# Kernel optimization log

Hardware: AMD Instinct MI355X
Metric: run time of the kernel (lower is better)

## Reference

```python
import jax, jax.numpy as jnp
import numpy as np
import math

DROPOUT_P = 0.1

def setup_inputs() -> dict:
    key = jax.random.key(0)
    k1, k2, k3 = jax.random.split(key, 3)
    B, Lq, Lk, D = 8, 2048, 2048, 128
    x1 = jax.random.normal(k1, (B, Lq, D), dtype=jnp.float32)
    x2 = jax.random.normal(k2, (B, Lk, D), dtype=jnp.float32)
    qm = jnp.zeros((1, Lq, Lk), dtype=jnp.float32)  # additive attention mask
    u = jax.random.uniform(k3, (B, Lq, Lk), dtype=jnp.float32)  # dropout uniforms
    return {"x1": x1, "x2": x2, "qm": qm, "u": u}

def reference(x1, x2, qm, u):
    # scaled dot-product attention with additive mask + inverted dropout
    scale = 1.0 / math.sqrt(x1.shape[-1])
    qk = jnp.einsum('bqd,bkd->bqk', x1, x2) * scale + qm  # [B, Lq, Lk]
    attn = jax.nn.softmax(qk, axis=-1)
    keep = (u >= DROPOUT_P).astype(attn.dtype) / (1.0 - DROPOUT_P)
    attn = attn * keep
    out = jnp.einsum('bqk,bkd->bqd', attn, x2)  # [B, Lq, D]
    return out
```

## Files before the change

### kernel.cpp

```cpp
#include <hip/hip_runtime.h>
#include <hip/hip_bf16.h>
#include <stdint.h>

#define LQ 2048
#define LK 2048
#define DH 128
#define BQ 64
#define KB 128
#define NT (LK / KB)
#define KROW 136
#define LOG2E 1.44269504088896340736f
#define QSCALE 0.088388347648318447f

typedef __attribute__((ext_vector_type(8)))  short bf16x8;
typedef __attribute__((ext_vector_type(16))) float f32x16;
typedef __attribute__((ext_vector_type(4)))  float f32x4;

union FragAB { uint32_t u[4]; bf16x8 v; };

__device__ __forceinline__ uint32_t pack2_bf16(float lo, float hi) {
  union { __hip_bfloat16 b; uint16_t u; } a, c;
  a.b = __float2bfloat16(lo);
  c.b = __float2bfloat16(hi);
  return (uint32_t)a.u | ((uint32_t)c.u << 16);
}

__device__ __forceinline__ void stage_writes(uint16_t* Kb, uint16_t* Vb,
                                             const f32x4* st, int sbi, int sbj) {
#pragma unroll
  for (int j = 0; j < 2; ++j) {
    const int rowb = 4 * (sbi + 16 * j);
#pragma unroll
    for (int r = 0; r < 4; ++r) {
      uint32_t* kw = (uint32_t*)(Kb + (size_t)(rowb + r) * KROW + 4 * sbj);
      f32x4 v = st[j * 4 + r];
      kw[0] = pack2_bf16(v.x, v.y);
      kw[1] = pack2_bf16(v.z, v.w);
    }
#pragma unroll
    for (int c = 0; c < 4; ++c) {
      uint32_t* vw = (uint32_t*)(Vb + (size_t)(4 * sbj + c) * KROW + rowb);
      vw[0] = pack2_bf16(st[j * 4 + 0][c], st[j * 4 + 1][c]);
      vw[1] = pack2_bf16(st[j * 4 + 2][c], st[j * 4 + 3][c]);
    }
  }
}

__global__ __launch_bounds__(512, 2)
void fattn_kernel(const float* __restrict__ x1, const float* __restrict__ x2,
                  const float* __restrict__ qm, const float* __restrict__ uu,
                  float* __restrict__ out)
{
  __shared__ uint16_t ldsK[2][128 * KROW];
  __shared__ uint16_t ldsV[2][128 * KROW];

  const int tid  = threadIdx.x;
  const int wv   = tid >> 6;
  const int lane = tid & 63;
  const int ln   = lane & 31;
  const int h    = lane >> 5;
  const int qsub = wv & 1;
  const int ks   = wv >> 1;

  const int b    = blockIdx.x & 7;
  const int qblk = blockIdx.x >> 3;
  const int qrow = qblk * BQ + qsub * 32 + ln;

  FragAB qf[8];
  {
    const float* qp = x1 + ((size_t)(b * LQ + qrow)) * DH + h * 8;
    const float qs = QSCALE * LOG2E;
#pragma unroll
    for (int dc = 0; dc < 8; ++dc) {
      f32x4 a = *(const f32x4*)(qp + dc * 16);
      f32x4 c = *(const f32x4*)(qp + dc * 16 + 4);
      qf[dc].u[0] = pack2_bf16(a.x * qs, a.y * qs);
      qf[dc].u[1] = pack2_bf16(a.z * qs, a.w * qs);
      qf[dc].u[2] = pack2_bf16(c.x * qs, c.y * qs);
      qf[dc].u[3] = pack2_bf16(c.z * qs, c.w * qs);
    }
  }

  const int sbi = tid >> 5;
  const int sbj = tid & 31;
  const float* x2base = x2 + (size_t)b * LK * DH + sbj * 4;
  const float* ubase  = uu + ((size_t)(b * LQ + qrow)) * LK + ks * 32 + h * 4;
  const float* qmbase = qm + ((size_t)qrow) * LK + ks * 32 + h * 4;

  f32x4 st[8];
#pragma unroll
  for (int j = 0; j < 2; ++j)
#pragma unroll
    for (int r = 0; r < 4; ++r)
      st[j * 4 + r] = *(const f32x4*)(x2base + (size_t)(4 * (sbi + 16 * j) + r) * DH);

  f32x4 ucur[4];
#pragma unroll
  for (int g = 0; g < 4; ++g)
    ucur[g] = __builtin_nontemporal_load((const f32x4*)(ubase + g * 8));

  stage_writes(ldsK[0], ldsV[0], st, sbi, sbj);
  __syncthreads();

  float m_run = -1e30f, l_run = 0.f;
  f32x16 acco[4];
#pragma unroll
  for (int d2 = 0; d2 < 4; ++d2)
#pragma unroll
    for (int i = 0; i < 16; ++i) acco[d2][i] = 0.f;

  for (int t = 0; t < NT; ++t) {
    const int cb = t & 1;
    const uint16_t* Kb = ldsK[cb];
    const uint16_t* Vb = ldsV[cb];
    const int kb = t * KB;

    f32x4 qmv[4];
#pragma unroll
    for (int g = 0; g < 4; ++g)
      qmv[g] = *(const f32x4*)(qmbase + (size_t)kb + g * 8);

    f32x4 unext[4];
    if (t + 1 < NT) {
#pragma unroll
      for (int j = 0; j < 2; ++j)
#pragma unroll
        for (int r = 0; r < 4; ++r)
          st[j * 4 + r] = *(const f32x4*)(x2base + (size_t)(kb + KB + 4 * (sbi + 16 * j) + r) * DH);
#pragma unroll
      for (int g = 0; g < 4; ++g)
        unext[g] = __builtin_nontemporal_load((const f32x4*)(ubase + (size_t)(kb + KB) + g * 8));
    }

    f32x16 sacc;
#pragma unroll
    for (int i = 0; i < 16; ++i) sacc[i] = 0.f;
    const uint16_t* Krow = Kb + (size_t)(ks * 32 + ln) * KROW + h * 8;
#pragma unroll
    for (int dc = 0; dc < 8; ++dc) {
      bf16x8 af = *(const bf16x8*)(Krow + dc * 16);
      sacc = __builtin_amdgcn_mfma_f32_32x32x16_bf16(af, qf[dc].v, sacc, 0, 0, 0);
    }

#pragma unroll
    for (int g = 0; g < 4; ++g)
#pragma unroll
      for (int j2 = 0; j2 < 4; ++j2)
        sacc[g * 4 + j2] += qmv[g][j2] * LOG2E;
    float pm = sacc[0];
#pragma unroll
    for (int i = 1; i < 16; ++i) pm = fmaxf(pm, sacc[i]);
    pm = fmaxf(pm, __shfl_xor(pm, 32));
    const float mnew = fmaxf(m_run, pm);
    const float resc = __builtin_amdgcn_exp2f(m_run - mnew);
    m_run = mnew;
    float rs = 0.f;
#pragma unroll
    for (int i = 0; i < 16; ++i) {
      sacc[i] = __builtin_amdgcn_exp2f(sacc[i] - mnew);
      rs += sacc[i];
    }
    rs += __shfl_xor(rs, 32);
    l_run = l_run * resc + rs;

#pragma unroll
    for (int g = 0; g < 4; ++g)
#pragma unroll
      for (int j2 = 0; j2 < 4; ++j2)
        sacc[g * 4 + j2] = (ucur[g][j2] >= 0.1f) ? sacc[g * 4 + j2] : 0.f;

    uint32_t pr[4][2], sw[4][2];
#pragma unroll
    for (int g = 0; g < 4; ++g) {
      pr[g][0] = pack2_bf16(sacc[4 * g + 0], sacc[4 * g + 1]);
      pr[g][1] = pack2_bf16(sacc[4 * g + 2], sacc[4 * g + 3]);
      sw[g][0] = __shfl_xor(pr[g][0], 32);
      sw[g][1] = __shfl_xor(pr[g][1], 32);
    }
    FragAB bfr[2];
#pragma unroll
    for (int c = 0; c < 2; ++c) {
      bfr[c].u[0] = h ? sw[2 * c + 1][0] : pr[2 * c][0];
      bfr[c].u[1] = h ? sw[2 * c + 1][1] : pr[2 * c][1];
      bfr[c].u[2] = h ? pr[2 * c + 1][0] : sw[2 * c][0];
      bfr[c].u[3] = h ? pr[2 * c + 1][1] : sw[2 * c][1];
    }

#pragma unroll
    for (int d2 = 0; d2 < 4; ++d2)
#pragma unroll
      for (int i = 0; i < 16; ++i) acco[d2][i] *= resc;

#pragma unroll
    for (int d2 = 0; d2 < 4; ++d2) {
      const uint16_t* Vrow = Vb + (size_t)(d2 * 32 + ln) * KROW + ks * 32 + h * 8;
#pragma unroll
      for (int c = 0; c < 2; ++c) {
        bf16x8 av = *(const bf16x8*)(Vrow + c * 16);
        acco[d2] = __builtin_amdgcn_mfma_f32_32x32x16_bf16(av, bfr[c].v, acco[d2], 0, 0, 0);
      }
    }

    if (t + 1 < NT) {
      stage_writes(ldsK[cb ^ 1], ldsV[cb ^ 1], st, sbi, sbj);
#pragma unroll
      for (int g = 0; g < 4; ++g) ucur[g] = unext[g];
    }
    __syncthreads();
  }

  float* scr = (wv < 4) ? ((float*)ldsK + (size_t)wv * 4224)
                        : ((float*)ldsV + (size_t)(wv - 4) * 4224);
  scr[lane]      = m_run;
  scr[64 + lane] = l_run;
#pragma unroll
  for (int d2 = 0; d2 < 4; ++d2)
#pragma unroll
    for (int g = 0; g < 4; ++g) {
      f32x4 vv;
#pragma unroll
      for (int j2 = 0; j2 < 4; ++j2) vv[j2] = acco[d2][g * 4 + j2];
      *(f32x4*)(scr + 128 + (size_t)(d2 * 4 + g) * 256 + lane * 4) = vv;
    }
  __syncthreads();

  if (wv < 2) {
    const float* rg[4];
#pragma unroll
    for (int s2 = 0; s2 < 4; ++s2) {
      const int r = qsub + 2 * s2;
      rg[s2] = (r < 4) ? ((const float*)ldsK + (size_t)r * 4224)
                       : ((const float*)ldsV + (size_t)(r - 4) * 4224);
    }
    const float ms0 = rg[0][lane], ms1 = rg[1][lane], ms2 = rg[2][lane], ms3 = rg[3][lane];
    const float ls0 = rg[0][64 + lane], ls1 = rg[1][64 + lane];
    const float ls2 = rg[2][64 + lane], ls3 = rg[3][64 + lane];
    const float mM = fmaxf(fmaxf(ms0, ms1), fmaxf(ms2, ms3));
    const float e0 = __builtin_amdgcn_exp2f(ms0 - mM);
    const float e1 = __builtin_amdgcn_exp2f(ms1 - mM);
    const float e2 = __builtin_amdgcn_exp2f(ms2 - mM);
    const float e3 = __builtin_amdgcn_exp2f(ms3 - mM);
    const float lM = e0 * ls0 + e1 * ls1 + e2 * ls2 + e3 * ls3;
    const float inv = (1.0f / 0.9f) / lM;
    float* op = out + ((size_t)(b * LQ + qrow)) * DH;
#pragma unroll
    for (int d2 = 0; d2 < 4; ++d2)
#pragma unroll
      for (int g = 0; g < 4; ++g) {
        const size_t off = 128 + (size_t)(d2 * 4 + g) * 256 + lane * 4;
        f32x4 a4 = e0 * *(const f32x4*)(rg[0] + off)
                 + e1 * *(const f32x4*)(rg[1] + off)
                 + e2 * *(const f32x4*)(rg[2] + off)
                 + e3 * *(const f32x4*)(rg[3] + off);
        a4 = a4 * inv;
        *(f32x4*)(op + d2 * 32 + 8 * g + 4 * h) = a4;
      }
  }
}

extern "C" void kernel_launch(void* const* d_in, const int* in_sizes, int n_in,
                              void* d_out, int out_size, void* d_ws, size_t ws_size,
                              hipStream_t stream) {
  (void)in_sizes; (void)n_in; (void)out_size; (void)d_ws; (void)ws_size;
  const float* x1 = (const float*)d_in[0];
  const float* x2 = (const float*)d_in[1];
  const float* qm = (const float*)d_in[2];
  const float* u  = (const float*)d_in[3];
  float* out = (float*)d_out;
  dim3 grid(256), block(512);
  fattn_kernel<<<grid, block, 0, stream>>>(x1, x2, qm, u, out);
}
```

Before: 257.5 us.

## Precompute dropout bitmask and bf16 transposed mask in prepass kernels

Two new prepass kernels run before attention. One packs the float dropout uniforms into a bit mask using wave ballots, and the other converts the additive mask into pre-scaled bf16 in a transposed layout matched to the MFMA fragments. The attention kernel then reads a single 32-bit word per tile for dropout and two 16-byte loads for the mask, replacing many scattered fp32 loads in the inner loop. The cost is two extra launches and a full read of the uniforms tensor in the prepass. Separately, the LDS staging writes are merged into 64-bit stores, and the mask is rounded to bf16, which loses some precision.

```diff
diff --git a/kernel.cpp b/kernel.cpp
--- a/kernel.cpp
+++ b/kernel.cpp
@@ -25,6 +25,58 @@
   return (uint32_t)a.u | ((uint32_t)c.u << 16);
 }
 
+__global__ __launch_bounds__(256)
+void mask_kernel(const float* __restrict__ uu, uint32_t* __restrict__ maskp) {
+  const int lane = threadIdx.x & 63;
+  const int wid  = blockIdx.x * 4 + (threadIdx.x >> 6);
+#pragma unroll 1
+  for (int i = 0; i < 16; ++i) {
+    const size_t F = ((size_t)i * 8192 + wid) * 256;
+    float u0 = uu[F + 0 * 64 + lane];
+    float u1 = uu[F + 1 * 64 + lane];
+    float u2 = uu[F + 2 * 64 + lane];
+    float u3 = uu[F + 3 * 64 + lane];
+    uint64_t B0 = __ballot(u0 >= 0.1f);
+    uint64_t B1 = __ballot(u1 >= 0.1f);
+    uint64_t B2 = __ballot(u2 >= 0.1f);
+    uint64_t B3 = __ballot(u3 >= 0.1f);
+    if (lane < 8) {
+      const int m = lane;
+      uint64_t bb = (m < 2) ? B0 : (m < 4) ? B1 : (m < 6) ? B2 : B3;
+      uint32_t val = (m & 1) ? (uint32_t)(bb >> 32) : (uint32_t)bb;
+      const size_t row = F >> 11;
+      const int c = (int)((F >> 5) & 63) + m;
+      maskp[row * 64 + (size_t)((c & 3) * 16 + (c >> 2))] = val;
+    }
+  }
+}
+
+__global__ __launch_bounds__(256)
+void qmt_kernel(const float* __restrict__ qm, uint16_t* __restrict__ qmt2) {
+  const int kc = threadIdx.x & 63;
+  const int q  = blockIdx.x * 4 + (threadIdx.x >> 6);
+  f32x4 r[8];
+  const float* src = qm + (size_t)q * 2048 + kc * 32;
+#pragma unroll
+  for (int c = 0; c < 8; ++c) r[c] = *(const f32x4*)(src + c * 4);
+#pragma unroll
+  for (int h = 0; h < 2; ++h) {
+    uint32_t w[8];
+#pragma unroll
+    for (int i = 0; i < 8; ++i) {
+      const int gi0 = 2 * i, gi1 = 2 * i + 1;
+      const float v0 = r[h + (gi0 >> 2) * 2][gi0 & 3] * LOG2E;
+      const float v1 = r[h + (gi1 >> 2) * 2][gi1 & 3] * LOG2E;
+      w[i] = pack2_bf16(v0, v1);
+    }
+    uint16_t* dst = qmt2 + ((size_t)(kc * 2 + h) * 2048 + q) * 16;
+    uint4 lo = {w[0], w[1], w[2], w[3]};
+    uint4 hi = {w[4], w[5], w[6], w[7]};
+    *(uint4*)dst = lo;
+    *(uint4*)(dst + 8) = hi;
+  }
+}
+
 __device__ __forceinline__ void stage_writes(uint16_t* Kb, uint16_t* Vb,
                                              const f32x4* st, int sbi, int sbj) {
 #pragma unroll
@@ -32,23 +84,24 @@
     const int rowb = 4 * (sbi + 16 * j);
 #pragma unroll
     for (int r = 0; r < 4; ++r) {
-      uint32_t* kw = (uint32_t*)(Kb + (size_t)(rowb + r) * KROW + 4 * sbj);
       f32x4 v = st[j * 4 + r];
-      kw[0] = pack2_bf16(v.x, v.y);
-      kw[1] = pack2_bf16(v.z, v.w);
+      uint64_t pk = (uint64_t)pack2_bf16(v.x, v.y) |
+                    ((uint64_t)pack2_bf16(v.z, v.w) << 32);
+      *(uint64_t*)(Kb + (size_t)(rowb + r) * KROW + 4 * sbj) = pk;
     }
 #pragma unroll
     for (int c = 0; c < 4; ++c) {
-      uint32_t* vw = (uint32_t*)(Vb + (size_t)(4 * sbj + c) * KROW + rowb);
-      vw[0] = pack2_bf16(st[j * 4 + 0][c], st[j * 4 + 1][c]);
-      vw[1] = pack2_bf16(st[j * 4 + 2][c], st[j * 4 + 3][c]);
+      uint64_t pv = (uint64_t)pack2_bf16(st[j * 4 + 0][c], st[j * 4 + 1][c]) |
+                    ((uint64_t)pack2_bf16(st[j * 4 + 2][c], st[j * 4 + 3][c]) << 32);
+      *(uint64_t*)(Vb + (size_t)(4 * sbj + c) * KROW + rowb) = pv;
     }
   }
 }
 
 __global__ __launch_bounds__(512, 2)
 void fattn_kernel(const float* __restrict__ x1, const float* __restrict__ x2,
-                  const float* __restrict__ qm, const float* __restrict__ uu,
+                  const uint32_t* __restrict__ maskp,
+                  const uint16_t* __restrict__ qmt2,
                   float* __restrict__ out)
 {
   __shared__ uint16_t ldsK[2][128 * KROW];
@@ -84,8 +137,7 @@
   const int sbi = tid >> 5;
   const int sbj = tid & 31;
   const float* x2base = x2 + (size_t)b * LK * DH + sbj * 4;
-  const float* ubase  = uu + ((size_t)(b * LQ + qrow)) * LK + ks * 32 + h * 4;
-  const float* qmbase = qm + ((size_t)qrow) * LK + ks * 32 + h * 4;
+  const uint32_t* maskrow = maskp + ((size_t)(b * LQ + qrow)) * 64 + ks * 16;
 
   f32x4 st[8];
 #pragma unroll
@@ -94,10 +146,13 @@
     for (int r = 0; r < 4; ++r)
       st[j * 4 + r] = *(const f32x4*)(x2base + (size_t)(4 * (sbi + 16 * j) + r) * DH);
 
-  f32x4 ucur[4];
-#pragma unroll
-  for (int g = 0; g < 4; ++g)
-    ucur[g] = __builtin_nontemporal_load((const f32x4*)(ubase + g * 8));
+  uint32_t mcur = maskrow[0];
+  uint4 qc0, qc1;
+  {
+    const uint16_t* qp16 = qmt2 + (((size_t)(0 * 4 + ks) * 2 + h) * 2048 + qrow) * 16;
+    qc0 = *(const uint4*)qp16;
+    qc1 = *(const uint4*)(qp16 + 8);
+  }
 
   stage_writes(ldsK[0], ldsV[0], st, sbi, sbj);
   __syncthreads();
@@ -115,21 +170,17 @@
     const uint16_t* Vb = ldsV[cb];
     const int kb = t * KB;
 
-    f32x4 qmv[4];
-#pragma unroll
-    for (int g = 0; g < 4; ++g)
-      qmv[g] = *(const f32x4*)(qmbase + (size_t)kb + g * 8);
-
-    f32x4 unext[4];
+    uint32_t mnxt = 0; uint4 qn0, qn1;
     if (t + 1 < NT) {
 #pragma unroll
       for (int j = 0; j < 2; ++j)
 #pragma unroll
         for (int r = 0; r < 4; ++r)
           st[j * 4 + r] = *(const f32x4*)(x2base + (size_t)(kb + KB + 4 * (sbi + 16 * j) + r) * DH);
-#pragma unroll
-      for (int g = 0; g < 4; ++g)
-        unext[g] = __builtin_nontemporal_load((const f32x4*)(ubase + (size_t)(kb + KB) + g * 8));
+      mnxt = maskrow[t + 1];
+      const uint16_t* qp16 = qmt2 + (((size_t)((t + 1) * 4 + ks) * 2 + h) * 2048 + qrow) * 16;
+      qn0 = *(const uint4*)qp16;
+      qn1 = *(const uint4*)(qp16 + 8);
     }
 
     f32x16 sacc;
@@ -142,11 +193,12 @@
       sacc = __builtin_amdgcn_mfma_f32_32x32x16_bf16(af, qf[dc].v, sacc, 0, 0, 0);
     }
 
-#pragma unroll
-    for (int g = 0; g < 4; ++g)
-#pragma unroll
-      for (int j2 = 0; j2 < 4; ++j2)
-        sacc[g * 4 + j2] += qmv[g][j2] * LOG2E;
+#define ADDQM(W, I) { sacc[I] += __uint_as_float((W) << 16); \
+                      sacc[I + 1] += __uint_as_float((W) & 0xffff0000u); }
+    ADDQM(qc0.x, 0)  ADDQM(qc0.y, 2)  ADDQM(qc0.z, 4)  ADDQM(qc0.w, 6)
+    ADDQM(qc1.x, 8)  ADDQM(qc1.y, 10) ADDQM(qc1.z, 12) ADDQM(qc1.w, 14)
+#undef ADDQM
+
     float pm = sacc[0];
 #pragma unroll
     for (int i = 1; i < 16; ++i) pm = fmaxf(pm, sacc[i]);
@@ -166,8 +218,10 @@
 #pragma unroll
     for (int g = 0; g < 4; ++g)
 #pragma unroll
-      for (int j2 = 0; j2 < 4; ++j2)
-        sacc[g * 4 + j2] = (ucur[g][j2] >= 0.1f) ? sacc[g * 4 + j2] : 0.f;
+      for (int j2 = 0; j2 < 4; ++j2) {
+        const uint32_t keep = (mcur >> (h * 4 + g * 8 + j2)) & 1u;
+        sacc[g * 4 + j2] = keep ? sacc[g * 4 + j2] : 0.f;
+      }
 
     uint32_t pr[4][2], sw[4][2];
 #pragma unroll
@@ -203,8 +257,7 @@
 
     if (t + 1 < NT) {
       stage_writes(ldsK[cb ^ 1], ldsV[cb ^ 1], st, sbi, sbj);
-#pragma unroll
-      for (int g = 0; g < 4; ++g) ucur[g] = unext[g];
+      mcur = mnxt; qc0 = qn0; qc1 = qn1;
     }
     __syncthreads();
   }
@@ -261,12 +314,17 @@
 extern "C" void kernel_launch(void* const* d_in, const int* in_sizes, int n_in,
                               void* d_out, int out_size, void* d_ws, size_t ws_size,
                               hipStream_t stream) {
-  (void)in_sizes; (void)n_in; (void)out_size; (void)d_ws; (void)ws_size;
+  (void)in_sizes; (void)n_in; (void)out_size; (void)ws_size;
   const float* x1 = (const float*)d_in[0];
   const float* x2 = (const float*)d_in[1];
   const float* qm = (const float*)d_in[2];
   const float* u  = (const float*)d_in[3];
   float* out = (float*)d_out;
-  dim3 grid(256), block(512);
-  fattn_kernel<<<grid, block, 0, stream>>>(x1, x2, qm, u, out);
-}
+
+  uint32_t* maskp = (uint32_t*)d_ws;
+  uint16_t* qmt2  = (uint16_t*)((char*)d_ws + (4u << 20));
+
+  mask_kernel<<<dim3(2048), dim3(256), 0, stream>>>(u, maskp);
+  qmt_kernel<<<dim3(512), dim3(256), 0, stream>>>(qm, qmt2);
+  fattn_kernel<<<dim3(256), dim3(512), 0, stream>>>(x1, x2, maskp, qmt2, out);
+}
```

New measurement: 269.5 us. 1.05x slower.
